# Performance work log

Hardware: AMD Instinct MI355X
Metric: run time of the kernel (lower is better)

The kernel has to match this reference:

```python
import jax, jax.numpy as jnp
import numpy as np

N_NODES = 50000
N_EDGES = 1600000
NODE_DIM = 64
HID = 16


def setup_inputs() -> dict:
    key = jax.random.key(0)
    ks = jax.random.split(key, 12)
    f = lambda k, shape: (jax.random.normal(k, shape, dtype=jnp.float32) * 0.1)
    edge_index = jax.random.randint(ks[0], (2, N_EDGES), 0, N_NODES)
    return {
        "edge_index": edge_index,
        "node_emb": f(ks[1], (N_NODES, NODE_DIM)),
        "edge_emb": f(ks[2], (N_EDGES, HID)),
        "W1": f(ks[3], (NODE_DIM, HID)),
        "att_src1": f(ks[4], (HID,)),
        "att_dst1": f(ks[5], (HID,)),
        "b1": jnp.zeros((HID,), jnp.float32),
        "W2": f(ks[6], (HID, HID)),
        "att_src2": f(ks[7], (HID,)),
        "att_dst2": f(ks[8], (HID,)),
        "b2": jnp.zeros((HID,), jnp.float32),
        "Wm1": f(ks[9], (3 * HID, HID)),
        "bm1": jnp.zeros((HID,), jnp.float32),
        "Wm2": f(ks[10], (HID, 1)),
        "bm2": jnp.zeros((1,), jnp.float32),
    }


def gat_layer(x, src, dst, W, a_src, a_dst, b, num_nodes):
    # Single-head GATConv (PyG defaults): self-loops, leaky_relu(0.2), softmax over dst.
    h = x @ W  # [N, out]
    logits = jax.nn.leaky_relu((h @ a_src)[src] + (h @ a_dst)[dst], negative_slope=0.2)
    m = jax.ops.segment_max(logits, dst, num_segments=num_nodes)  # stable softmax
    e = jnp.exp(logits - jax.lax.stop_gradient(m)[dst])
    denom = jax.ops.segment_sum(e, dst, num_segments=num_nodes)
    coef = e / denom[dst]  # [E+N]
    out = jax.ops.segment_sum(coef[:, None] * h[src], dst, num_segments=num_nodes)
    return out + b


def reference(edge_index, node_emb, edge_emb, W1, att_src1, att_dst1, b1,
              W2, att_src2, att_dst2, b2, Wm1, bm1, Wm2, bm2):
    src, dst = edge_index[0], edge_index[1]
    num_nodes = node_emb.shape[0]
    loops = jnp.arange(num_nodes)
    src_f = jnp.concatenate([src, loops])  # GATConv add_self_loops=True
    dst_f = jnp.concatenate([dst, loops])

    x = node_emb
    for (W, a_s, a_d, b) in [(W1, att_src1, att_dst1, b1), (W2, att_src2, att_dst2, b2)]:
        x = gat_layer(x, src_f, dst_f, W, a_s, a_d, b, num_nodes)
        x = jax.nn.gelu(x, approximate=False)  # torch F.gelu default = exact erf
        # dropout omitted (eval mode)

    # Vectorized replacement of the per-edge Python loop:
    edge_repr = jnp.concatenate([x[src], x[dst], edge_emb], axis=1)  # [E, 3*HID]
    hmid = jax.nn.relu(edge_repr @ Wm1 + bm1)
    probs = jax.nn.sigmoid(hmid @ Wm2 + bm2)[:, 0]  # [E]
    return probs
```

## Files before the change

### kernel.cpp

```cpp
#include <hip/hip_runtime.h>
#include <math.h>
#include <string.h>

#define N_NODES 50000
#define N_EDGES 1600000
#define NODE_DIM 64
#define HID 16
#define BSZ 64
#define NBUCK ((N_NODES + BSZ - 1) / BSZ)
#define CAPB 2560
#define EPB 2048
#define APB 256
#define APPEND_BLOCKS ((N_EDGES + EPB - 1) / EPB)

typedef _Float16 h8 __attribute__((ext_vector_type(8)));

__global__ void append_kernel(const int* __restrict__ ei,
                              int* __restrict__ gcount,
                              unsigned int* __restrict__ blist) {
    __shared__ int lcount[NBUCK];
    __shared__ int gbase[NBUCK];
    __shared__ int loff[NBUCK];
    int t = threadIdx.x;
    for (int b = t; b < NBUCK; b += APB) { lcount[b] = 0; loff[b] = 0; }
    __syncthreads();
    long base = (long)blockIdx.x * EPB;
#pragma unroll
    for (int k = 0; k < EPB / APB; k++) {
        long i = base + k * APB + t;
        if (i < N_EDGES) atomicAdd(&lcount[ei[N_EDGES + i] >> 6], 1);
    }
    __syncthreads();
    for (int b = t; b < NBUCK; b += APB) {
        int c = lcount[b];
        gbase[b] = c ? atomicAdd(&gcount[b], c) : 0;
    }
    __syncthreads();
#pragma unroll
    for (int k = 0; k < EPB / APB; k++) {
        long i = base + k * APB + t;
        if (i < N_EDGES) {
            int s = ei[i], d = ei[N_EDGES + i];
            int b = d >> 6;
            int pos = gbase[b] + atomicAdd(&loff[b], 1);
            if (pos < CAPB)
                blist[(size_t)b * CAPB + pos] = ((unsigned)(d & 63) << 16) | (unsigned)s;
        }
    }
}

__global__ void sort_kernel(const int* __restrict__ gcount, const unsigned int* __restrict__ blist,
                            unsigned short* __restrict__ csr, int* __restrict__ dstbeg) {
    __shared__ int cnts[BSZ];
    __shared__ int sc[BSZ];
    __shared__ int off[BSZ];
    int b = blockIdx.x, t = threadIdx.x;
    if (t < BSZ) cnts[t] = 0;
    __syncthreads();
    int cnt = gcount[b]; if (cnt > CAPB) cnt = CAPB;
    const unsigned int* lp = blist + (size_t)b * CAPB;
    for (int k = t; k < cnt; k += APB) atomicAdd(&cnts[lp[k] >> 16], 1);
    __syncthreads();
    if (t < BSZ) sc[t] = cnts[t];
    __syncthreads();
    for (int o = 1; o < BSZ; o <<= 1) {
        int v = 0;
        if (t < BSZ && t >= o) v = sc[t - o];
        __syncthreads();
        if (t < BSZ) sc[t] += v;
        __syncthreads();
    }
    if (t < BSZ) {
        int beg = sc[t] - cnts[t];
        off[t] = beg;
        dstbeg[(b << 6) + t] = beg;
    }
    __syncthreads();
    for (int k = t; k < cnt; k += APB) {
        unsigned int r = lp[k];
        int pos = atomicAdd(&off[r >> 16], 1);
        csr[(size_t)b * CAPB + pos] = (unsigned short)(r & 0xFFFF);
    }
}

__global__ void node_h64(const float* __restrict__ x,
                         const float* __restrict__ W,
                         const float* __restrict__ a_src,
                         const float* __restrict__ a_dst,
                         _Float16* __restrict__ h16,
                         float* __restrict__ as_, float* __restrict__ ad_,
                         int* __restrict__ gcount) {
    int t = threadIdx.x;
    int n = blockIdx.x * blockDim.x + t;
    if (n < NBUCK) gcount[n] = 0;
    if (n >= N_NODES) return;
    float acc[HID];
#pragma unroll
    for (int j = 0; j < HID; j++) acc[j] = 0.f;
    const float4* xr = (const float4*)(x + (size_t)n * NODE_DIM);
#pragma unroll
    for (int k4 = 0; k4 < NODE_DIM / 4; k4++) {
        float4 xv = xr[k4];
        const float* w0 = W + (k4 * 4) * HID;
#pragma unroll
        for (int j = 0; j < HID; j++)
            acc[j] += xv.x * w0[j] + xv.y * w0[HID + j] + xv.z * w0[2 * HID + j] + xv.w * w0[3 * HID + j];
    }
    float s = 0.f, d = 0.f;
#pragma unroll
    for (int j = 0; j < HID; j++) {
        s += acc[j] * a_src[j];
        d += acc[j] * a_dst[j];
    }
    h8 hv0, hv1;
#pragma unroll
    for (int j = 0; j < 8; j++) { hv0[j] = (_Float16)acc[j]; hv1[j] = (_Float16)acc[8 + j]; }
    h8* hp = (h8*)(h16 + (size_t)n * HID);
    hp[0] = hv0; hp[1] = hv1;
    as_[n] = s; ad_[n] = d;
}

__device__ __forceinline__ void gather_core(
        const unsigned short* __restrict__ row, int cnt, int j,
        const _Float16* __restrict__ h16, const float* __restrict__ as_, float adn,
        float& acc, float& den) {
    int k = 0;
    for (; k + 4 <= cnt; k += 4) {
        int s0 = row[k], s1 = row[k + 1], s2 = row[k + 2], s3 = row[k + 3];
        float l0 = as_[s0] + adn, l1 = as_[s1] + adn;
        float l2 = as_[s2] + adn, l3 = as_[s3] + adn;
        l0 = l0 > 0.f ? l0 : 0.2f * l0;
        l1 = l1 > 0.f ? l1 : 0.2f * l1;
        l2 = l2 > 0.f ? l2 : 0.2f * l2;
        l3 = l3 > 0.f ? l3 : 0.2f * l3;
        float e0 = expf(l0), e1 = expf(l1), e2 = expf(l2), e3 = expf(l3);
        float h0 = (float)h16[(size_t)s0 * HID + j];
        float h1 = (float)h16[(size_t)s1 * HID + j];
        float h2 = (float)h16[(size_t)s2 * HID + j];
        float h3 = (float)h16[(size_t)s3 * HID + j];
        den += (e0 + e1) + (e2 + e3);
        acc += (e0 * h0 + e1 * h1) + (e2 * h2 + e3 * h3);
    }
    for (; k < cnt; k++) {
        int s = row[k];
        float lg = as_[s] + adn;
        lg = lg > 0.f ? lg : 0.2f * lg;
        float e = expf(lg);
        den += e;
        acc += e * (float)h16[(size_t)s * HID + j];
    }
}

__global__ void gather1_fused(const int* __restrict__ gcount, const int* __restrict__ dstbeg,
                              const unsigned short* __restrict__ csr,
                              const _Float16* __restrict__ h1,
                              const float* __restrict__ as_, const float* __restrict__ ad_,
                              const float* __restrict__ b,
                              const float* __restrict__ W2,
                              const float* __restrict__ a_src2,
                              const float* __restrict__ a_dst2,
                              _Float16* __restrict__ h2,
                              float* __restrict__ as2, float* __restrict__ ad2) {
    int t = threadIdx.x;
    int j = t & 15;
    float Wcol[HID];
#pragma unroll
    for (int k = 0; k < HID; k++) Wcol[k] = W2[k * HID + j];
    float a2j = a_src2[j], d2j = a_dst2[j], bj = b[j];
    int g = blockIdx.x * (blockDim.x >> 4) + (t >> 4);
    if (g >= N_NODES) return;
    int bk = g >> 6, dl = g & 63;
    int cnt_b = gcount[bk]; if (cnt_b > CAPB) cnt_b = CAPB;
    int beg = dstbeg[g];
    int end = (dl < 63) ? dstbeg[g + 1] : cnt_b;
    if (end > cnt_b) end = cnt_b;
    if (beg > end) beg = end;
    const unsigned short* row = csr + (size_t)bk * CAPB + beg;
    float adn = ad_[g];
    float acc = 0.f, den = 0.f;
    gather_core(row, end - beg, j, h1, as_, adn, acc, den);
    float lg = as_[g] + adn;
    lg = lg > 0.f ? lg : 0.2f * lg;
    float e = expf(lg);
    den += e;
    acc += e * (float)h1[(size_t)g * HID + j];
    float v = acc / den + bj;
    v = 0.5f * v * (1.f + erff(v * 0.70710678118654752f));
    float acc2 = 0.f;
#pragma unroll
    for (int k2 = 0; k2 < HID; k2++) {
        float xk = __shfl(v, k2, 16);
        acc2 += xk * Wcol[k2];
    }
    float ps = acc2 * a2j, pd = acc2 * d2j;
#pragma unroll
    for (int o = 1; o < 16; o <<= 1) {
        ps += __shfl_xor(ps, o, 16);
        pd += __shfl_xor(pd, o, 16);
    }
    h2[(size_t)g * HID + j] = (_Float16)acc2;
    if (j == 0) { as2[g] = ps; ad2[g] = pd; }
}

__global__ void gather2_fused(const int* __restrict__ gcount, const int* __restrict__ dstbeg,
                              const unsigned short* __restrict__ csr,
                              const _Float16* __restrict__ h2,
                              const float* __restrict__ as_, const float* __restrict__ ad_,
                              const float* __restrict__ b,
                              const float* __restrict__ Wm1,
                              const float* __restrict__ bm1,
                              _Float16* __restrict__ A, _Float16* __restrict__ B) {
    int t = threadIdx.x;
    int j = t & 15;
    float WaC[HID], WbC[HID];
#pragma unroll
    for (int k = 0; k < HID; k++) {
        WaC[k] = Wm1[k * HID + j];
        WbC[k] = Wm1[HID * HID + k * HID + j];
    }
    float bj = b[j], b1j = bm1[j];
    int g = blockIdx.x * (blockDim.x >> 4) + (t >> 4);
    if (g >= N_NODES) return;
    int bk = g >> 6, dl = g & 63;
    int cnt_b = gcount[bk]; if (cnt_b > CAPB) cnt_b = CAPB;
    int beg = dstbeg[g];
    int end = (dl < 63) ? dstbeg[g + 1] : cnt_b;
    if (end > cnt_b) end = cnt_b;
    if (beg > end) beg = end;
    const unsigned short* row = csr + (size_t)bk * CAPB + beg;
    float adn = ad_[g];
    float acc = 0.f, den = 0.f;
    gather_core(row, end - beg, j, h2, as_, adn, acc, den);
    float lg = as_[g] + adn;
    lg = lg > 0.f ? lg : 0.2f * lg;
    float e = expf(lg);
    den += e;
    acc += e * (float)h2[(size_t)g * HID + j];
    float v = acc / den + bj;
    v = 0.5f * v * (1.f + erff(v * 0.70710678118654752f));
    float accA = b1j, accB = 0.f;
#pragma unroll
    for (int k2 = 0; k2 < HID; k2++) {
        float xk = __shfl(v, k2, 16);
        accA += xk * WaC[k2];
        accB += xk * WbC[k2];
    }
    A[(size_t)g * HID + j] = (_Float16)accA;
    B[(size_t)g * HID + j] = (_Float16)accB;
}

__global__ void edge_mlp(const int* __restrict__ ei,
                         const _Float16* __restrict__ A,
                         const _Float16* __restrict__ B,
                         const float* __restrict__ ee,
                         const float* __restrict__ Wm1,
                         const float* __restrict__ Wm2,
                         const float* __restrict__ bm2,
                         float* __restrict__ out) {
    int t = threadIdx.x;
    long i = (long)blockIdx.x * blockDim.x + t;
    if (i >= N_EDGES) return;
    int s = ei[i], d = ei[N_EDGES + i];
    const h8* Ap = (const h8*)(A + (size_t)s * HID);
    const h8* Bp = (const h8*)(B + (size_t)d * HID);
    h8 a0 = Ap[0], a1 = Ap[1];
    h8 b0 = Bp[0], b1 = Bp[1];
    const float4* ep = (const float4*)(ee + (size_t)i * HID);
    float4 e0 = ep[0], e1 = ep[1], e2 = ep[2], e3 = ep[3];
    float a[HID];
#pragma unroll
    for (int j = 0; j < 8; j++) {
        a[j]     = (float)a0[j] + (float)b0[j];
        a[8 + j] = (float)a1[j] + (float)b1[j];
    }
    float ev[HID];
    ev[0]  = e0.x; ev[1]  = e0.y; ev[2]  = e0.z; ev[3]  = e0.w;
    ev[4]  = e1.x; ev[5]  = e1.y; ev[6]  = e1.z; ev[7]  = e1.w;
    ev[8]  = e2.x; ev[9]  = e2.y; ev[10] = e2.z; ev[11] = e2.w;
    ev[12] = e3.x; ev[13] = e3.y; ev[14] = e3.z; ev[15] = e3.w;
    const float4* W4 = (const float4*)(Wm1 + 2 * HID * HID);
#pragma unroll
    for (int k = 0; k < HID; k++) {
        float e1v = ev[k];
        float4 w0 = W4[k * 4 + 0], w1 = W4[k * 4 + 1], w2 = W4[k * 4 + 2], w3 = W4[k * 4 + 3];
        a[0]  += e1v * w0.x; a[1]  += e1v * w0.y; a[2]  += e1v * w0.z; a[3]  += e1v * w0.w;
        a[4]  += e1v * w1.x; a[5]  += e1v * w1.y; a[6]  += e1v * w1.z; a[7]  += e1v * w1.w;
        a[8]  += e1v * w2.x; a[9]  += e1v * w2.y; a[10] += e1v * w2.z; a[11] += e1v * w2.w;
        a[12] += e1v * w3.x; a[13] += e1v * w3.y; a[14] += e1v * w3.z; a[15] += e1v * w3.w;
    }
    float o = bm2[0];
#pragma unroll
    for (int j = 0; j < HID; j++) o += fmaxf(a[j], 0.f) * Wm2[j];
    out[i] = 1.f / (1.f + expf(-o));
}

extern "C" void kernel_launch(void* const* d_in, const int* in_sizes, int n_in,
                              void* d_out, int out_size, void* d_ws, size_t ws_size,
                              hipStream_t stream) {
    const int*   ei       = (const int*)d_in[0];
    const float* node_emb = (const float*)d_in[1];
    const float* edge_emb = (const float*)d_in[2];
    const float* W1       = (const float*)d_in[3];
    const float* att_src1 = (const float*)d_in[4];
    const float* att_dst1 = (const float*)d_in[5];
    const float* b1       = (const float*)d_in[6];
    const float* W2       = (const float*)d_in[7];
    const float* att_src2 = (const float*)d_in[8];
    const float* att_dst2 = (const float*)d_in[9];
    const float* b2       = (const float*)d_in[10];
    const float* Wm1      = (const float*)d_in[11];
    const float* bm1      = (const float*)d_in[12];
    const float* Wm2      = (const float*)d_in[13];
    const float* bm2      = (const float*)d_in[14];
    float* out            = (float*)d_out;

    char* w = (char*)d_ws;
    _Float16*       h1     = (_Float16*)w;       w += (size_t)N_NODES * HID * 2;
    _Float16*       h2     = (_Float16*)w;       w += (size_t)N_NODES * HID * 2;
    _Float16*       Anode  = (_Float16*)w;       w += (size_t)N_NODES * HID * 2;
    _Float16*       Bnode  = (_Float16*)w;       w += (size_t)N_NODES * HID * 2;
    float*          as1    = (float*)w;          w += (size_t)N_NODES * 4;
    float*          ad1    = (float*)w;          w += (size_t)N_NODES * 4;
    float*          as2    = (float*)w;          w += (size_t)N_NODES * 4;
    float*          ad2    = (float*)w;          w += (size_t)N_NODES * 4;
    int*            gcount = (int*)w;            w += (size_t)NBUCK * 4;
    unsigned int*   blist  = (unsigned int*)w;   w += (size_t)NBUCK * CAPB * 4;
    unsigned short* csr    = (unsigned short*)w; w += (size_t)NBUCK * CAPB * 2;
    int*            dstbeg = (int*)w;            w += (size_t)NBUCK * BSZ * 4;

    const int BT = 256;
    int nblk_node = (N_NODES + BT - 1) / BT;
    int nblk_E    = (N_EDGES + BT - 1) / BT;
    int nblk_g    = (N_NODES * HID + BT - 1) / BT;

    node_h64<<<nblk_node, BT, 0, stream>>>(node_emb, W1, att_src1, att_dst1,
                                           h1, as1, ad1, gcount);
    append_kernel<<<APPEND_BLOCKS, APB, 0, stream>>>(ei, gcount, blist);
    sort_kernel<<<NBUCK, APB, 0, stream>>>(gcount, blist, csr, dstbeg);

    gather1_fused<<<nblk_g, BT, 0, stream>>>(gcount, dstbeg, csr, h1, as1, ad1, b1,
                                             W2, att_src2, att_dst2, h2, as2, ad2);
    gather2_fused<<<nblk_g, BT, 0, stream>>>(gcount, dstbeg, csr, h2, as2, ad2, b2,
                                             Wm1, bm1, Anode, Bnode);

    edge_mlp<<<nblk_E, BT, 0, stream>>>(ei, Anode, Bnode, edge_emb, Wm1, Wm2, bm2, out);
}
```

Before: 340.3 us.

## Merge node projection into bucket-append kernel, unroll gather by 8, add launch bounds

The node feature projection kernel becomes extra blocks of the edge-bucketing kernel, so one launch does both jobs and the two independent pieces of work can overlap. The bucket counters are now cleared with a memset instead of inside the projection kernel. The gather inner loop is unrolled from 4 to 8 edges and all loads are issued before the math, to put more memory requests in flight. Launch bounds are added to the gather and edge MLP kernels, which may limit registers and cause spills.

```diff
diff --git a/kernel.cpp b/kernel.cpp
--- a/kernel.cpp
+++ b/kernel.cpp
@@ -12,40 +12,76 @@
 #define EPB 2048
 #define APB 256
 #define APPEND_BLOCKS ((N_EDGES + EPB - 1) / EPB)
+#define NODE_BLOCKS ((N_NODES + APB - 1) / APB)
 
 typedef _Float16 h8 __attribute__((ext_vector_type(8)));
 
-__global__ void append_kernel(const int* __restrict__ ei,
-                              int* __restrict__ gcount,
-                              unsigned int* __restrict__ blist) {
+__global__ void build_kernel(const int* __restrict__ ei,
+                             int* __restrict__ gcount,
+                             unsigned int* __restrict__ blist,
+                             const float* __restrict__ x,
+                             const float* __restrict__ W,
+                             const float* __restrict__ a_src,
+                             const float* __restrict__ a_dst,
+                             _Float16* __restrict__ h16,
+                             float* __restrict__ as_, float* __restrict__ ad_) {
     __shared__ int lcount[NBUCK];
     __shared__ int gbase[NBUCK];
     __shared__ int loff[NBUCK];
     int t = threadIdx.x;
-    for (int b = t; b < NBUCK; b += APB) { lcount[b] = 0; loff[b] = 0; }
-    __syncthreads();
-    long base = (long)blockIdx.x * EPB;
-#pragma unroll
-    for (int k = 0; k < EPB / APB; k++) {
-        long i = base + k * APB + t;
-        if (i < N_EDGES) atomicAdd(&lcount[ei[N_EDGES + i] >> 6], 1);
-    }
-    __syncthreads();
-    for (int b = t; b < NBUCK; b += APB) {
-        int c = lcount[b];
-        gbase[b] = c ? atomicAdd(&gcount[b], c) : 0;
-    }
-    __syncthreads();
-#pragma unroll
-    for (int k = 0; k < EPB / APB; k++) {
-        long i = base + k * APB + t;
-        if (i < N_EDGES) {
-            int s = ei[i], d = ei[N_EDGES + i];
-            int b = d >> 6;
-            int pos = gbase[b] + atomicAdd(&loff[b], 1);
-            if (pos < CAPB)
-                blist[(size_t)b * CAPB + pos] = ((unsigned)(d & 63) << 16) | (unsigned)s;
-        }
+    if (blockIdx.x < APPEND_BLOCKS) {
+        for (int b = t; b < NBUCK; b += APB) { lcount[b] = 0; loff[b] = 0; }
+        __syncthreads();
+        long base = (long)blockIdx.x * EPB;
+#pragma unroll
+        for (int k = 0; k < EPB / APB; k++) {
+            long i = base + k * APB + t;
+            if (i < N_EDGES) atomicAdd(&lcount[ei[N_EDGES + i] >> 6], 1);
+        }
+        __syncthreads();
+        for (int b = t; b < NBUCK; b += APB) {
+            int c = lcount[b];
+            gbase[b] = c ? atomicAdd(&gcount[b], c) : 0;
+        }
+        __syncthreads();
+#pragma unroll
+        for (int k = 0; k < EPB / APB; k++) {
+            long i = base + k * APB + t;
+            if (i < N_EDGES) {
+                int s = ei[i], d = ei[N_EDGES + i];
+                int b = d >> 6;
+                int pos = gbase[b] + atomicAdd(&loff[b], 1);
+                if (pos < CAPB)
+                    blist[(size_t)b * CAPB + pos] = ((unsigned)(d & 63) << 16) | (unsigned)s;
+            }
+        }
+    } else {
+        int n = (blockIdx.x - APPEND_BLOCKS) * APB + t;
+        if (n >= N_NODES) return;
+        float acc[HID];
+#pragma unroll
+        for (int j = 0; j < HID; j++) acc[j] = 0.f;
+        const float4* xr = (const float4*)(x + (size_t)n * NODE_DIM);
+#pragma unroll
+        for (int k4 = 0; k4 < NODE_DIM / 4; k4++) {
+            float4 xv = xr[k4];
+            const float* w0 = W + (k4 * 4) * HID;
+#pragma unroll
+            for (int j = 0; j < HID; j++)
+                acc[j] += xv.x * w0[j] + xv.y * w0[HID + j] + xv.z * w0[2 * HID + j] + xv.w * w0[3 * HID + j];
+        }
+        float s = 0.f, d = 0.f;
+#pragma unroll
+        for (int j = 0; j < HID; j++) {
+            s += acc[j] * a_src[j];
+            d += acc[j] * a_dst[j];
+        }
+        h8 hv0, hv1;
+#pragma unroll
+        for (int j = 0; j < 8; j++) { hv0[j] = (_Float16)acc[j]; hv1[j] = (_Float16)acc[8 + j]; }
+        h8* hp = (h8*)(h16 + (size_t)n * HID);
+        hp[0] = hv0; hp[1] = hv1;
+        as_[n] = s; ad_[n] = d;
     }
 }
 
@@ -83,63 +119,35 @@
     }
 }
 
-__global__ void node_h64(const float* __restrict__ x,
-                         const float* __restrict__ W,
-                         const float* __restrict__ a_src,
-                         const float* __restrict__ a_dst,
-                         _Float16* __restrict__ h16,
-                         float* __restrict__ as_, float* __restrict__ ad_,
-                         int* __restrict__ gcount) {
-    int t = threadIdx.x;
-    int n = blockIdx.x * blockDim.x + t;
-    if (n < NBUCK) gcount[n] = 0;
-    if (n >= N_NODES) return;
-    float acc[HID];
-#pragma unroll
-    for (int j = 0; j < HID; j++) acc[j] = 0.f;
-    const float4* xr = (const float4*)(x + (size_t)n * NODE_DIM);
-#pragma unroll
-    for (int k4 = 0; k4 < NODE_DIM / 4; k4++) {
-        float4 xv = xr[k4];
-        const float* w0 = W + (k4 * 4) * HID;
-#pragma unroll
-        for (int j = 0; j < HID; j++)
-            acc[j] += xv.x * w0[j] + xv.y * w0[HID + j] + xv.z * w0[2 * HID + j] + xv.w * w0[3 * HID + j];
-    }
-    float s = 0.f, d = 0.f;
-#pragma unroll
-    for (int j = 0; j < HID; j++) {
-        s += acc[j] * a_src[j];
-        d += acc[j] * a_dst[j];
-    }
-    h8 hv0, hv1;
-#pragma unroll
-    for (int j = 0; j < 8; j++) { hv0[j] = (_Float16)acc[j]; hv1[j] = (_Float16)acc[8 + j]; }
-    h8* hp = (h8*)(h16 + (size_t)n * HID);
-    hp[0] = hv0; hp[1] = hv1;
-    as_[n] = s; ad_[n] = d;
-}
-
 __device__ __forceinline__ void gather_core(
         const unsigned short* __restrict__ row, int cnt, int j,
         const _Float16* __restrict__ h16, const float* __restrict__ as_, float adn,
         float& acc, float& den) {
     int k = 0;
-    for (; k + 4 <= cnt; k += 4) {
-        int s0 = row[k], s1 = row[k + 1], s2 = row[k + 2], s3 = row[k + 3];
-        float l0 = as_[s0] + adn, l1 = as_[s1] + adn;
-        float l2 = as_[s2] + adn, l3 = as_[s3] + adn;
-        l0 = l0 > 0.f ? l0 : 0.2f * l0;
-        l1 = l1 > 0.f ? l1 : 0.2f * l1;
-        l2 = l2 > 0.f ? l2 : 0.2f * l2;
-        l3 = l3 > 0.f ? l3 : 0.2f * l3;
-        float e0 = expf(l0), e1 = expf(l1), e2 = expf(l2), e3 = expf(l3);
+    for (; k + 8 <= cnt; k += 8) {
+        int s0 = row[k],     s1 = row[k + 1], s2 = row[k + 2], s3 = row[k + 3];
+        int s4 = row[k + 4], s5 = row[k + 5], s6 = row[k + 6], s7 = row[k + 7];
+        float a0 = as_[s0], a1 = as_[s1], a2 = as_[s2], a3 = as_[s3];
+        float a4 = as_[s4], a5 = as_[s5], a6 = as_[s6], a7 = as_[s7];
         float h0 = (float)h16[(size_t)s0 * HID + j];
         float h1 = (float)h16[(size_t)s1 * HID + j];
         float h2 = (float)h16[(size_t)s2 * HID + j];
         float h3 = (float)h16[(size_t)s3 * HID + j];
-        den += (e0 + e1) + (e2 + e3);
-        acc += (e0 * h0 + e1 * h1) + (e2 * h2 + e3 * h3);
+        float h4 = (float)h16[(size_t)s4 * HID + j];
+        float h5 = (float)h16[(size_t)s5 * HID + j];
+        float h6 = (float)h16[(size_t)s6 * HID + j];
+        float h7 = (float)h16[(size_t)s7 * HID + j];
+        float l0 = a0 + adn, l1 = a1 + adn, l2 = a2 + adn, l3 = a3 + adn;
+        float l4 = a4 + adn, l5 = a5 + adn, l6 = a6 + adn, l7 = a7 + adn;
+        l0 = l0 > 0.f ? l0 : 0.2f * l0;  l1 = l1 > 0.f ? l1 : 0.2f * l1;
+        l2 = l2 > 0.f ? l2 : 0.2f * l2;  l3 = l3 > 0.f ? l3 : 0.2f * l3;
+        l4 = l4 > 0.f ? l4 : 0.2f * l4;  l5 = l5 > 0.f ? l5 : 0.2f * l5;
+        l6 = l6 > 0.f ? l6 : 0.2f * l6;  l7 = l7 > 0.f ? l7 : 0.2f * l7;
+        float e0 = expf(l0), e1 = expf(l1), e2 = expf(l2), e3 = expf(l3);
+        float e4 = expf(l4), e5 = expf(l5), e6 = expf(l6), e7 = expf(l7);
+        den += ((e0 + e1) + (e2 + e3)) + ((e4 + e5) + (e6 + e7));
+        acc += ((e0 * h0 + e1 * h1) + (e2 * h2 + e3 * h3))
+             + ((e4 * h4 + e5 * h5) + (e6 * h6 + e7 * h7));
     }
     for (; k < cnt; k++) {
         int s = row[k];
@@ -151,16 +159,17 @@
     }
 }
 
-__global__ void gather1_fused(const int* __restrict__ gcount, const int* __restrict__ dstbeg,
-                              const unsigned short* __restrict__ csr,
-                              const _Float16* __restrict__ h1,
-                              const float* __restrict__ as_, const float* __restrict__ ad_,
-                              const float* __restrict__ b,
-                              const float* __restrict__ W2,
-                              const float* __restrict__ a_src2,
-                              const float* __restrict__ a_dst2,
-                              _Float16* __restrict__ h2,
-                              float* __restrict__ as2, float* __restrict__ ad2) {
+__global__ __launch_bounds__(256, 4)
+void gather1_fused(const int* __restrict__ gcount, const int* __restrict__ dstbeg,
+                   const unsigned short* __restrict__ csr,
+                   const _Float16* __restrict__ h1,
+                   const float* __restrict__ as_, const float* __restrict__ ad_,
+                   const float* __restrict__ b,
+                   const float* __restrict__ W2,
+                   const float* __restrict__ a_src2,
+                   const float* __restrict__ a_dst2,
+                   _Float16* __restrict__ h2,
+                   float* __restrict__ as2, float* __restrict__ ad2) {
     int t = threadIdx.x;
     int j = t & 15;
     float Wcol[HID];
@@ -202,14 +211,15 @@
     if (j == 0) { as2[g] = ps; ad2[g] = pd; }
 }
 
-__global__ void gather2_fused(const int* __restrict__ gcount, const int* __restrict__ dstbeg,
-                              const unsigned short* __restrict__ csr,
-                              const _Float16* __restrict__ h2,
-                              const float* __restrict__ as_, const float* __restrict__ ad_,
-                              const float* __restrict__ b,
-                              const float* __restrict__ Wm1,
-                              const float* __restrict__ bm1,
-                              _Float16* __restrict__ A, _Float16* __restrict__ B) {
+__global__ __launch_bounds__(256, 4)
+void gather2_fused(const int* __restrict__ gcount, const int* __restrict__ dstbeg,
+                   const unsigned short* __restrict__ csr,
+                   const _Float16* __restrict__ h2,
+                   const float* __restrict__ as_, const float* __restrict__ ad_,
+                   const float* __restrict__ b,
+                   const float* __restrict__ Wm1,
+                   const float* __restrict__ bm1,
+                   _Float16* __restrict__ A, _Float16* __restrict__ B) {
     int t = threadIdx.x;
     int j = t & 15;
     float WaC[HID], WbC[HID];
@@ -249,23 +259,24 @@
     B[(size_t)g * HID + j] = (_Float16)accB;
 }
 
-__global__ void edge_mlp(const int* __restrict__ ei,
-                         const _Float16* __restrict__ A,
-                         const _Float16* __restrict__ B,
-                         const float* __restrict__ ee,
-                         const float* __restrict__ Wm1,
-                         const float* __restrict__ Wm2,
-                         const float* __restrict__ bm2,
-                         float* __restrict__ out) {
+__global__ __launch_bounds__(256, 4)
+void edge_mlp(const int* __restrict__ ei,
+              const _Float16* __restrict__ A,
+              const _Float16* __restrict__ B,
+              const float* __restrict__ ee,
+              const float* __restrict__ Wm1,
+              const float* __restrict__ Wm2,
+              const float* __restrict__ bm2,
+              float* __restrict__ out) {
     int t = threadIdx.x;
     long i = (long)blockIdx.x * blockDim.x + t;
     if (i >= N_EDGES) return;
     int s = ei[i], d = ei[N_EDGES + i];
     const h8* Ap = (const h8*)(A + (size_t)s * HID);
     const h8* Bp = (const h8*)(B + (size_t)d * HID);
+    const float4* ep = (const float4*)(ee + (size_t)i * HID);
     h8 a0 = Ap[0], a1 = Ap[1];
     h8 b0 = Bp[0], b1 = Bp[1];
-    const float4* ep = (const float4*)(ee + (size_t)i * HID);
     float4 e0 = ep[0], e1 = ep[1], e2 = ep[2], e3 = ep[3];
     float a[HID];
 #pragma unroll
@@ -329,13 +340,12 @@
     int*            dstbeg = (int*)w;            w += (size_t)NBUCK * BSZ * 4;
 
     const int BT = 256;
-    int nblk_node = (N_NODES + BT - 1) / BT;
     int nblk_E    = (N_EDGES + BT - 1) / BT;
     int nblk_g    = (N_NODES * HID + BT - 1) / BT;
 
-    node_h64<<<nblk_node, BT, 0, stream>>>(node_emb, W1, att_src1, att_dst1,
-                                           h1, as1, ad1, gcount);
-    append_kernel<<<APPEND_BLOCKS, APB, 0, stream>>>(ei, gcount, blist);
+    hipMemsetAsync(gcount, 0, (size_t)NBUCK * sizeof(int), stream);
+    build_kernel<<<APPEND_BLOCKS + NODE_BLOCKS, APB, 0, stream>>>(
+        ei, gcount, blist, node_emb, W1, att_src1, att_dst1, h1, as1, ad1);
     sort_kernel<<<NBUCK, APB, 0, stream>>>(gcount, blist, csr, dstbeg);
 
     gather1_fused<<<nblk_g, BT, 0, stream>>>(gcount, dstbeg, csr, h1, as1, ad1, b1,
```

Result: no change. 336.1 us (-1.2%).
